# Optimization experiments

Hardware: AMD Instinct MI355X
Metric: run time of the kernel (lower is better)

## Reference

```python
import jax, jax.numpy as jnp
import numpy as np

IN_DIM, OUT_DIM = 1024, 1024
GRID_SIZE, K = 8, 3
TOKENS = 8192


def b_splines(x, grid, k):
    # x: [B, in_dim], grid: [in_dim, grid_size + 2k + 1]
    x = x[..., None]  # [B, in_dim, 1]
    # order-0 indicator bases: [B, in_dim, grid_size + 2k]
    bases = ((x >= grid[:, :-1]) & (x < grid[:, 1:])).astype(x.dtype)
    # Cox-de Boor recursion up to order k -> [B, in_dim, grid_size + k]
    for kk in range(1, k + 1):
        left = (x - grid[:, : -(kk + 1)]) / (grid[:, kk:-1] - grid[:, : -(kk + 1)])
        right = (grid[:, kk + 1:] - x) / (grid[:, kk + 1:] - grid[:, 1:-kk])
        bases = left * bases[..., :-1] + right * bases[..., 1:]
    return bases


def setup_inputs() -> dict:
    key = jax.random.key(0)
    k1, k2, k3 = jax.random.split(key, 3)
    x = jax.random.normal(k1, (TOKENS, IN_DIM), dtype=jnp.float32)
    # grid buffer: arange(-k, grid_size+k+1) * step + grid_range[0], repeated per in_dim
    grid_range = (-1.0, 1.0)
    step = (grid_range[1] - grid_range[0]) / GRID_SIZE
    grid_row = np.arange(-K, GRID_SIZE + K + 1, dtype=np.float32) * step + grid_range[0]
    grid = jnp.asarray(np.tile(grid_row, (IN_DIM, 1)))  # [in_dim, 15]
    coeff = jax.random.normal(k2, (OUT_DIM, IN_DIM, GRID_SIZE + K), dtype=jnp.float32) * 0.1
    scale_base = 1.0 / np.sqrt(IN_DIM) + jax.random.normal(k3, (OUT_DIM, IN_DIM), dtype=jnp.float32) * 0.1
    scale_spline = jnp.ones((1,), dtype=jnp.float32)
    return {"x": x, "grid": grid, "coeff": coeff, "scale_base": scale_base,
            "scale_spline": scale_spline}


def reference(x, grid, coeff, scale_base, scale_spline):
    splines = b_splines(x, grid, K)                      # [B, in, G+K]
    y_b = jnp.matmul(jax.nn.silu(x), scale_base.T)       # [B, out]
    w = coeff * scale_spline                             # scalar broadcast [out, in, G+K]
    y_spline = jnp.einsum('big,oig->bo', splines, w)     # [B, out]
    return y_b + y_spline
```

## Files before the change

### kernel.cpp

```cpp
#include <hip/hip_runtime.h>
#include <hip/hip_bf16.h>
#include <stdint.h>

typedef __attribute__((ext_vector_type(8))) short short8;
typedef __attribute__((ext_vector_type(16))) float floatx16;
typedef unsigned short u16;

#define IN_DIM  1024
#define OUT_DIM 1024
#define NG      11
#define GK      12
#define KDIM    (IN_DIM * GK)
#define TOKENS  8192
#define BK      64

__device__ __forceinline__ u16 f2bf(float f) {
  uint32_t u = __float_as_uint(f);
  uint32_t r = (u + 0x7fffu + ((u >> 16) & 1u)) >> 16;
  return (u16)r;
}

__global__ __launch_bounds__(256) void pack_wt_kernel(
    const float* __restrict__ coeff, const float* __restrict__ sb,
    const float* __restrict__ ss_p, u16* __restrict__ Wt)
{
  __shared__ float cf[256 * NG];
  __shared__ __align__(16) u16 st[256 * GK];
  const int tid = threadIdx.x;
  const int b   = blockIdx.x;
  const int o   = b >> 2;
  const int i0  = (b & 3) * 256;
  const float* cbase = coeff + (size_t)o * (IN_DIM * NG) + (size_t)i0 * NG;
#pragma unroll
  for (int p = 0; p < NG; ++p) cf[p * 256 + tid] = cbase[p * 256 + tid];
  const float ss  = ss_p[0];
  const float sbv = sb[(size_t)o * IN_DIM + i0 + tid];
  __syncthreads();
  const float* cp = cf + tid * NG;
  u16 h[GK];
#pragma unroll
  for (int g = 0; g < NG; ++g) h[g] = f2bf(cp[g] * ss);
  h[NG] = f2bf(sbv);
  uint64_t V0 = (uint64_t)h[0] | ((uint64_t)h[1] << 16) | ((uint64_t)h[2] << 32) | ((uint64_t)h[3] << 48);
  uint64_t V1 = (uint64_t)h[4] | ((uint64_t)h[5] << 16) | ((uint64_t)h[6] << 32) | ((uint64_t)h[7] << 48);
  uint64_t V2 = (uint64_t)h[8] | ((uint64_t)h[9] << 16) | ((uint64_t)h[10] << 32) | ((uint64_t)h[11] << 48);
  uint64_t* sp = (uint64_t*)(st + tid * GK);
  sp[0] = V0; sp[1] = V1; sp[2] = V2;
  __syncthreads();
  const uint4* src = (const uint4*)st;
  uint4* dst = (uint4*)(Wt + (size_t)b * (256 * GK));
  dst[tid] = src[tid];
  if (tid < 128) dst[256 + tid] = src[256 + tid];
}

__global__ __launch_bounds__(256) void expand_kernel(
    const float* __restrict__ X, const float* __restrict__ grid,
    u16* __restrict__ A, int m0)
{
  __shared__ __align__(16) u16 st[256 * GK];
  int tid = threadIdx.x;
  int idx = blockIdx.x * 256 + tid;
  float x = X[(size_t)m0 * IN_DIM + idx];

  const float g0    = grid[0];
  const float inv_h = 1.0f / (grid[1] - grid[0]);

  float t  = (x - g0) * inv_h;
  float fc = floorf(t);
  int   c  = (int)fc;
  float u  = t - fc;
  float u2 = u * u;
  float w1 = 1.0f - u;
  float b0 = (w1 * w1 * w1) * (1.0f / 6.0f);
  float b1 = (0.5f * u - 1.0f) * u2 + (2.0f / 3.0f);
  float b2 = ((-0.5f * u + 0.5f) * u + 0.5f) * u + (1.0f / 6.0f);
  float b3 = (u2 * u) * (1.0f / 6.0f);
  float sil = x / (1.0f + __expf(-x));

  uint64_t P = (uint64_t)f2bf(b0) | ((uint64_t)f2bf(b1) << 16)
             | ((uint64_t)f2bf(b2) << 32) | ((uint64_t)f2bf(b3) << 48);
  int  k  = c - 3;
  bool cv = (c >= 0) && (c <= 13);
  int  kneg = (k < 0) ? -k : 0;
  uint64_t Pc = cv ? (P >> (16 * kneg)) : 0ull;
  uint32_t sh = (uint32_t)(16 * ((k < 0) ? 0 : k));

  uint64_t V0 = (sh < 64)  ? (Pc << (sh & 63)) : 0ull;
  uint64_t V1 = (sh == 0)  ? 0ull :
                (sh < 64)  ? (Pc >> ((64 - sh) & 63)) :
                (sh < 128) ? (Pc << ((sh - 64) & 63)) : 0ull;
  uint64_t V2 = (sh <= 64) ? 0ull :
                (sh < 128) ? (Pc >> ((128 - sh) & 63)) :
                             (Pc << ((sh - 128) & 63));
  V2 = (V2 & 0x0000FFFFFFFFFFFFull) | ((uint64_t)f2bf(sil) << 48);

  uint64_t* sp = (uint64_t*)(st + tid * GK);
  sp[0] = V0; sp[1] = V1; sp[2] = V2;
  __syncthreads();

  const uint4* src = (const uint4*)st;
  uint4* dst = (uint4*)(A + (size_t)blockIdx.x * (256 * GK));
  dst[tid] = src[tid];
  if (tid < 128) dst[256 + tid] = src[256 + tid];
}

__device__ __forceinline__ void async16(const u16* g, u16* l) {
  __builtin_amdgcn_global_load_lds(
      (const __attribute__((address_space(1))) uint32_t*)g,
      (__attribute__((address_space(3))) uint32_t*)l,
      16, 0, 0);
}

__global__ __launch_bounds__(256, 4) void gemm_kernel(
    const u16* __restrict__ A, const u16* __restrict__ Wt,
    float* __restrict__ out, float* __restrict__ part,
    int m0, int mtiles, int k_iters)
{
  __shared__ __align__(16) u16 As[128 * BK];
  __shared__ __align__(16) u16 Bs[128 * BK];

  const int tid  = threadIdx.x;
  const int lane = tid & 63;
  const int wave = tid >> 6;
  const int mt8  = mtiles * 8;
  const int s    = blockIdx.x / mt8;
  const int r    = blockIdx.x - s * mt8;
  const int bm   = r % mtiles;
  const int bn   = r / mtiles;
  const int kb   = s * k_iters * BK;
  const int wm = (wave >> 1) * 64;
  const int wn = (wave & 1) * 64;

  floatx16 acc[2][2];
#pragma unroll
  for (int a = 0; a < 2; ++a)
#pragma unroll
    for (int b = 0; b < 2; ++b)
#pragma unroll
      for (int rr = 0; rr < 16; ++rr) acc[a][b][rr] = 0.f;

  const int srow  = lane >> 3;
  const int gamma = (lane & 7) ^ srow;
  const u16* Ag = A  + (size_t)(bm * 128 + wave * 32 + srow) * KDIM + kb + gamma * 8;
  const u16* Bg = Wt + (size_t)(bn * 128 + wave * 32 + srow) * KDIM + kb + gamma * 8;
  u16* Al = As + (wave * 32) * BK;
  u16* Bl = Bs + (wave * 32) * BK;

  const int l31 = lane & 31;
  const int g   = lane >> 5;
  const int sw  = lane & 7;

  for (int it = 0; it < k_iters; ++it) {
    const int k0 = it * BK;
#pragma unroll
    for (int op = 0; op < 4; ++op) {
      async16(Ag + k0 + (size_t)(op * 8) * KDIM, Al + op * 8 * BK);
      async16(Bg + k0 + (size_t)(op * 8) * KDIM, Bl + op * 8 * BK);
    }
    __syncthreads();

#pragma unroll
    for (int t = 0; t < 4; ++t) {
      const int cc = (t * 2 + g) ^ sw;
      short8 af[2], bf[2];
#pragma unroll
      for (int ss = 0; ss < 2; ++ss) {
        af[ss] = *(const short8*)&As[(wm + ss * 32 + l31) * BK + cc * 8];
        bf[ss] = *(const short8*)&Bs[(wn + ss * 32 + l31) * BK + cc * 8];
      }
#pragma unroll
      for (int sm = 0; sm < 2; ++sm)
#pragma unroll
        for (int sn = 0; sn < 2; ++sn)
          acc[sm][sn] = __builtin_amdgcn_mfma_f32_32x32x16_bf16(af[sm], bf[sn], acc[sm][sn], 0, 0, 0);
    }

    __syncthreads();
  }

  float* op = (s == 0) ? out : part;
#pragma unroll
  for (int sm = 0; sm < 2; ++sm)
#pragma unroll
    for (int sn = 0; sn < 2; ++sn) {
      const int row0 = m0 + bm * 128 + wm + sm * 32 + 4 * g;
      const int col  = bn * 128 + wn + sn * 32 + l31;
#pragma unroll
      for (int reg = 0; reg < 16; ++reg) {
        int row = row0 + (reg & 3) + 8 * (reg >> 2);
        op[(size_t)row * OUT_DIM + col] = acc[sm][sn][reg];
      }
    }
}

__global__ __launch_bounds__(256) void reduce_kernel(
    float* __restrict__ out, const float* __restrict__ part)
{
  size_t i = (size_t)blockIdx.x * 256 + threadIdx.x;
  float4* o = (float4*)out;
  const float4* p = (const float4*)part;
  float4 a = o[i], b = p[i];
  a.x += b.x; a.y += b.y; a.z += b.z; a.w += b.w;
  o[i] = a;
}

extern "C" void kernel_launch(void* const* d_in, const int* in_sizes, int n_in,
                              void* d_out, int out_size, void* d_ws, size_t ws_size,
                              hipStream_t stream) {
  const float* x     = (const float*)d_in[0];
  const float* grid  = (const float*)d_in[1];
  const float* coeff = (const float*)d_in[2];
  const float* sb    = (const float*)d_in[3];
  const float* ss    = (const float*)d_in[4];
  float* out = (float*)d_out;

  u16* Wt = (u16*)d_ws;
  const size_t wt_bytes   = (size_t)OUT_DIM * KDIM * 2;
  const size_t a_bytes    = (size_t)TOKENS * KDIM * 2;
  const size_t part_bytes = (size_t)TOKENS * OUT_DIM * 4;
  u16*   Abuf = (u16*)((char*)d_ws + wt_bytes);
  float* part = (float*)((char*)d_ws + wt_bytes + a_bytes);

  pack_wt_kernel<<<(OUT_DIM * IN_DIM) / 256, 256, 0, stream>>>(coeff, sb, ss, Wt);

  if (ws_size >= wt_bytes + a_bytes + part_bytes) {
    expand_kernel<<<(TOKENS * IN_DIM) / 256, 256, 0, stream>>>(x, grid, Abuf, 0);
    gemm_kernel<<<64 * 8 * 2, 256, 0, stream>>>(Abuf, Wt, out, part, 0, 64, (KDIM / BK) / 2);
    reduce_kernel<<<(TOKENS * OUT_DIM / 4) / 256, 256, 0, stream>>>(out, part);
  } else {
    size_t avail   = ws_size > wt_bytes ? ws_size - wt_bytes : 0;
    size_t maxrows = avail / ((size_t)KDIM * 2);
    int chunk = (int)(maxrows & ~(size_t)127);
    if (chunk > TOKENS) chunk = TOKENS;
    if (chunk < 128)    chunk = 128;
    for (int m0 = 0; m0 < TOKENS; m0 += chunk) {
      int rows = TOKENS - m0 < chunk ? TOKENS - m0 : chunk;
      expand_kernel<<<(rows * IN_DIM) / 256, 256, 0, stream>>>(x, grid, Abuf, m0);
      gemm_kernel<<<(rows / 128) * 8, 256, 0, stream>>>(Abuf, Wt, out, nullptr, m0, rows / 128, KDIM / BK);
    }
  }
}
```

Before: 413.0 us.

## Fuse B-spline expansion into GEMM A-tile loading, drop expanded A buffer

The GEMM kernel now computes the bf16 B-spline/SiLU expansion of x in registers for each K-tile, instead of reading a precomputed 8192x12288 A buffer from global memory. This removes the separate expand kernel and its large write and reload. BK becomes 96 (8 input features per tile), and LDS rows are padded to 104 to replace the XOR swizzle. Weight tiles are now loaded through registers instead of async global-to-LDS copies. The cost is ALU work for the expansion inside the GEMM loop, more register pressure (occupancy hint lowered to 3), and no software prefetch overlap beyond register staging.

Result: slower. 668.5 us (+61.9%).

```diff
diff --git a/kernel.cpp b/kernel.cpp
--- a/kernel.cpp
+++ b/kernel.cpp
@@ -12,7 +12,9 @@
 #define GK      12
 #define KDIM    (IN_DIM * GK)
 #define TOKENS  8192
-#define BK      64
+#define MT      64
+#define BK      96
+#define PB      104
 
 __device__ __forceinline__ u16 f2bf(float f) {
   uint32_t u = __float_as_uint(f);
@@ -53,18 +55,9 @@
   if (tid < 128) dst[256 + tid] = src[256 + tid];
 }
 
-__global__ __launch_bounds__(256) void expand_kernel(
-    const float* __restrict__ X, const float* __restrict__ grid,
-    u16* __restrict__ A, int m0)
-{
-  __shared__ __align__(16) u16 st[256 * GK];
-  int tid = threadIdx.x;
-  int idx = blockIdx.x * 256 + tid;
-  float x = X[(size_t)m0 * IN_DIM + idx];
-
-  const float g0    = grid[0];
-  const float inv_h = 1.0f / (grid[1] - grid[0]);
-
+__device__ __forceinline__ void expand_regs(float x, float g0, float inv_h,
+                                            uint64_t& V0, uint64_t& V1, uint64_t& V2)
+{
   float t  = (x - g0) * inv_h;
   float fc = floorf(t);
   int   c  = (int)fc;
@@ -85,52 +78,38 @@
   uint64_t Pc = cv ? (P >> (16 * kneg)) : 0ull;
   uint32_t sh = (uint32_t)(16 * ((k < 0) ? 0 : k));
 
-  uint64_t V0 = (sh < 64)  ? (Pc << (sh & 63)) : 0ull;
-  uint64_t V1 = (sh == 0)  ? 0ull :
-                (sh < 64)  ? (Pc >> ((64 - sh) & 63)) :
-                (sh < 128) ? (Pc << ((sh - 64) & 63)) : 0ull;
-  uint64_t V2 = (sh <= 64) ? 0ull :
-                (sh < 128) ? (Pc >> ((128 - sh) & 63)) :
-                             (Pc << ((sh - 128) & 63));
+  V0 = (sh < 64)  ? (Pc << (sh & 63)) : 0ull;
+  V1 = (sh == 0)  ? 0ull :
+       (sh < 64)  ? (Pc >> ((64 - sh) & 63)) :
+       (sh < 128) ? (Pc << ((sh - 64) & 63)) : 0ull;
+  V2 = (sh <= 64) ? 0ull :
+       (sh < 128) ? (Pc >> ((128 - sh) & 63)) :
+                    (Pc << ((sh - 128) & 63));
   V2 = (V2 & 0x0000FFFFFFFFFFFFull) | ((uint64_t)f2bf(sil) << 48);
-
-  uint64_t* sp = (uint64_t*)(st + tid * GK);
-  sp[0] = V0; sp[1] = V1; sp[2] = V2;
-  __syncthreads();
-
-  const uint4* src = (const uint4*)st;
-  uint4* dst = (uint4*)(A + (size_t)blockIdx.x * (256 * GK));
-  dst[tid] = src[tid];
-  if (tid < 128) dst[256 + tid] = src[256 + tid];
-}
-
-__device__ __forceinline__ void async16(const u16* g, u16* l) {
-  __builtin_amdgcn_global_load_lds(
-      (const __attribute__((address_space(1))) uint32_t*)g,
-      (__attribute__((address_space(3))) uint32_t*)l,
-      16, 0, 0);
-}
-
-__global__ __launch_bounds__(256, 4) void gemm_kernel(
-    const u16* __restrict__ A, const u16* __restrict__ Wt,
-    float* __restrict__ out, float* __restrict__ part,
-    int m0, int mtiles, int k_iters)
-{
-  __shared__ __align__(16) u16 As[128 * BK];
-  __shared__ __align__(16) u16 Bs[128 * BK];
+}
+
+__global__ __launch_bounds__(256, 3) void gemm_fused_kernel(
+    const float* __restrict__ X, const float* __restrict__ grid,
+    const u16* __restrict__ Wt, float* __restrict__ out, float* __restrict__ part,
+    int k_iters)
+{
+  __shared__ __align__(16) u16 As[128 * PB];
+  __shared__ __align__(16) u16 Bs[128 * PB];
 
   const int tid  = threadIdx.x;
   const int lane = tid & 63;
   const int wave = tid >> 6;
-  const int mt8  = mtiles * 8;
+  const int mt8  = MT * 8;
   const int s    = blockIdx.x / mt8;
   const int r    = blockIdx.x - s * mt8;
-  const int bm   = r % mtiles;
-  const int bn   = r / mtiles;
-  const int kb   = s * k_iters * BK;
+  const int bm   = r % MT;
+  const int bn   = r / MT;
   const int wm = (wave >> 1) * 64;
   const int wn = (wave & 1) * 64;
 
+  const float g0    = grid[0];
+  const float inv_h = 1.0f / (grid[1] - grid[0]);
+
   floatx16 acc[2][2];
 #pragma unroll
   for (int a = 0; a < 2; ++a)
@@ -139,34 +118,60 @@
 #pragma unroll
       for (int rr = 0; rr < 16; ++rr) acc[a][b][rr] = 0.f;
 
-  const int srow  = lane >> 3;
-  const int gamma = (lane & 7) ^ srow;
-  const u16* Ag = A  + (size_t)(bm * 128 + wave * 32 + srow) * KDIM + kb + gamma * 8;
-  const u16* Bg = Wt + (size_t)(bn * 128 + wave * 32 + srow) * KDIM + kb + gamma * 8;
-  u16* Al = As + (wave * 32) * BK;
-  u16* Bl = Bs + (wave * 32) * BK;
+  const int kb_u16 = s * k_iters * BK;
+  const u16* bgp[6];
+  uint4*     blp[6];
+#pragma unroll
+  for (int j = 0; j < 6; ++j) {
+    int q  = tid + j * 256;
+    int rb = q / 12;
+    int cb = q - rb * 12;
+    bgp[j] = Wt + (size_t)(bn * 128 + rb) * KDIM + kb_u16 + cb * 8;
+    blp[j] = (uint4*)(Bs + rb * PB + cb * 8);
+  }
+
+  const int arow = tid & 127;
+  const int half = tid >> 7;
+  const float* xp = X + (size_t)(bm * 128 + arow) * IN_DIM + s * (k_iters * 8) + half * 4;
+  uint4* awp = (uint4*)(As + arow * PB + half * 48);
 
   const int l31 = lane & 31;
   const int g   = lane >> 5;
-  const int sw  = lane & 7;
 
   for (int it = 0; it < k_iters; ++it) {
-    const int k0 = it * BK;
-#pragma unroll
-    for (int op = 0; op < 4; ++op) {
-      async16(Ag + k0 + (size_t)(op * 8) * KDIM, Al + op * 8 * BK);
-      async16(Bg + k0 + (size_t)(op * 8) * KDIM, Bl + op * 8 * BK);
+    uint4 bv[6];
+#pragma unroll
+    for (int j = 0; j < 6; ++j) { bv[j] = *(const uint4*)bgp[j]; bgp[j] += BK; }
+
+    float4 xv = *(const float4*)(xp + it * 8);
+    uint64_t ev[12];
+    expand_regs(xv.x, g0, inv_h, ev[0], ev[1], ev[2]);
+    expand_regs(xv.y, g0, inv_h, ev[3], ev[4], ev[5]);
+    expand_regs(xv.z, g0, inv_h, ev[6], ev[7], ev[8]);
+    expand_regs(xv.w, g0, inv_h, ev[9], ev[10], ev[11]);
+
+    __syncthreads();
+
+#pragma unroll
+    for (int j = 0; j < 6; ++j) {
+      uint4 w;
+      w.x = (uint32_t)ev[2*j];     w.y = (uint32_t)(ev[2*j] >> 32);
+      w.z = (uint32_t)ev[2*j+1];   w.w = (uint32_t)(ev[2*j+1] >> 32);
+      awp[j] = w;
     }
+#pragma unroll
+    for (int j = 0; j < 6; ++j) *blp[j] = bv[j];
+
     __syncthreads();
 
 #pragma unroll
-    for (int t = 0; t < 4; ++t) {
-      const int cc = (t * 2 + g) ^ sw;
+    for (int t = 0; t < 6; ++t) {
+      const int cc = 2 * t + g;
       short8 af[2], bf[2];
 #pragma unroll
-      for (int ss = 0; ss < 2; ++ss) {
-        af[ss] = *(const short8*)&As[(wm + ss * 32 + l31) * BK + cc * 8];
-        bf[ss] = *(const short8*)&Bs[(wn + ss * 32 + l31) * BK + cc * 8];
+      for (int ss2 = 0; ss2 < 2; ++ss2) {
+        af[ss2] = *(const short8*)&As[(wm + ss2 * 32 + l31) * PB + cc * 8];
+        bf[ss2] = *(const short8*)&Bs[(wn + ss2 * 32 + l31) * PB + cc * 8];
       }
 #pragma unroll
       for (int sm = 0; sm < 2; ++sm)
@@ -174,16 +179,15 @@
         for (int sn = 0; sn < 2; ++sn)
           acc[sm][sn] = __builtin_amdgcn_mfma_f32_32x32x16_bf16(af[sm], bf[sn], acc[sm][sn], 0, 0, 0);
     }
-
-    __syncthreads();
   }
+  __syncthreads();
 
   float* op = (s == 0) ? out : part;
 #pragma unroll
   for (int sm = 0; sm < 2; ++sm)
 #pragma unroll
     for (int sn = 0; sn < 2; ++sn) {
-      const int row0 = m0 + bm * 128 + wm + sm * 32 + 4 * g;
+      const int row0 = bm * 128 + wm + sm * 32 + 4 * g;
       const int col  = bn * 128 + wn + sn * 32 + l31;
 #pragma unroll
       for (int reg = 0; reg < 16; ++reg) {
@@ -216,27 +220,15 @@
 
   u16* Wt = (u16*)d_ws;
   const size_t wt_bytes   = (size_t)OUT_DIM * KDIM * 2;
-  const size_t a_bytes    = (size_t)TOKENS * KDIM * 2;
   const size_t part_bytes = (size_t)TOKENS * OUT_DIM * 4;
-  u16*   Abuf = (u16*)((char*)d_ws + wt_bytes);
-  float* part = (float*)((char*)d_ws + wt_bytes + a_bytes);
+  float* part = (float*)((char*)d_ws + wt_bytes);
 
   pack_wt_kernel<<<(OUT_DIM * IN_DIM) / 256, 256, 0, stream>>>(coeff, sb, ss, Wt);
 
-  if (ws_size >= wt_bytes + a_bytes + part_bytes) {
-    expand_kernel<<<(TOKENS * IN_DIM) / 256, 256, 0, stream>>>(x, grid, Abuf, 0);
-    gemm_kernel<<<64 * 8 * 2, 256, 0, stream>>>(Abuf, Wt, out, part, 0, 64, (KDIM / BK) / 2);
+  if (ws_size >= wt_bytes + part_bytes) {
+    gemm_fused_kernel<<<MT * 8 * 2, 256, 0, stream>>>(x, grid, Wt, out, part, 64);
     reduce_kernel<<<(TOKENS * OUT_DIM / 4) / 256, 256, 0, stream>>>(out, part);
   } else {
-    size_t avail   = ws_size > wt_bytes ? ws_size - wt_bytes : 0;
-    size_t maxrows = avail / ((size_t)KDIM * 2);
-    int chunk = (int)(maxrows & ~(size_t)127);
-    if (chunk > TOKENS) chunk = TOKENS;
-    if (chunk < 128)    chunk = 128;
-    for (int m0 = 0; m0 < TOKENS; m0 += chunk) {
-      int rows = TOKENS - m0 < chunk ? TOKENS - m0 : chunk;
-      expand_kernel<<<(rows * IN_DIM) / 256, 256, 0, stream>>>(x, grid, Abuf, m0);
-      gemm_kernel<<<(rows / 128) * 8, 256, 0, stream>>>(Abuf, Wt, out, nullptr, m0, rows / 128, KDIM / BK);
-    }
+    gemm_fused_kernel<<<MT * 8, 256, 0, stream>>>(x, grid, Wt, out, nullptr, 128);
   }
 }
```
